# Kernel tuning notes

Hardware: AMD Instinct MI355X
Metric: run time of the kernel (lower is better)

Reference implementation:

```python
import jax, jax.numpy as jnp
import numpy as np

N_NODES = 100000
N_EDGES = 800000

def setup_inputs() -> dict:
    key = jax.random.key(0)
    ks = jax.random.split(key, 8)
    x = jax.random.normal(ks[0], (N_NODES, 500), dtype=jnp.float32)
    edge_index = jax.random.randint(ks[1], (2, N_EDGES), 0, N_NODES, dtype=jnp.int64)
    s = lambda k, shape, fan_in: jax.random.normal(k, shape, jnp.float32) / np.sqrt(fan_in)
    return {
        "x": x,
        "edge_index": edge_index,
        "W1_l": s(ks[2], (500, 20), 500),
        "W1_r": s(ks[3], (500, 20), 500),
        "b1": jnp.zeros((20,), jnp.float32),
        "W2_l": s(ks[4], (20, 3), 20),
        "W2_r": s(ks[5], (20, 3), 20),
        "b2": jnp.zeros((3,), jnp.float32),
    }

def _sage_conv(x, src, dst, W_l, W_r, b, deg_inv):
    # mean-aggregate neighbor features (x_j = x[src]) at dst, PyG default 'mean'
    agg = jax.ops.segment_sum(x[src], dst, num_segments=x.shape[0])  # [N, F]
    agg = agg * deg_inv[:, None]
    return agg @ W_l + b + x @ W_r

def reference(x, edge_index, W1_l, W1_r, b1, W2_l, W2_r, b2):
    src, dst = edge_index[0], edge_index[1]
    deg = jax.ops.segment_sum(jnp.ones_like(dst, dtype=x.dtype), dst, num_segments=x.shape[0])
    deg_inv = 1.0 / jnp.maximum(deg, 1.0)
    h = _sage_conv(x, src, dst, W1_l, W1_r, b1, deg_inv)
    h = jax.nn.relu(h)
    # F.dropout(p=0.5, training=self.training): identity in eval mode
    out = _sage_conv(h, src, dst, W2_l, W2_r, b2, deg_inv)
    return out
```

## Files before the change

kernel.cpp:

```cpp
#include <hip/hip_runtime.h>

#define F_IN  500
#define F_HID 20
#define F_OUT 3
#define KT    16
#define NT    3
#define PAD   32

typedef __attribute__((ext_vector_type(8))) short short8;
typedef __attribute__((ext_vector_type(4))) float v4f;

__device__ __forceinline__ unsigned f2bf(float f) {
    unsigned u = __float_as_uint(f);
    u = u + 0x7fffu + ((u >> 16) & 1u);
    return u >> 16;
}
__device__ __forceinline__ float bf2f(unsigned h) {
    return __uint_as_float(h << 16);
}

__device__ __forceinline__ void gload16(const void* g, void* l) {
    __builtin_amdgcn_global_load_lds((const __attribute__((address_space(1))) void*)g,
                                     (__attribute__((address_space(3))) void*)l, 16, 0, 0);
}

__device__ __forceinline__ void cvt8(const float4 p, const float4 q, short8& hi, short8& lo) {
    float vf[8] = {p.x, p.y, p.z, p.w, q.x, q.y, q.z, q.w};
    union { unsigned u[4]; short8 s; } H, L;
#pragma unroll
    for (int t = 0; t < 4; ++t) {
        unsigned u0 = __float_as_uint(vf[2*t]);
        unsigned u1 = __float_as_uint(vf[2*t+1]);
        unsigned r0 = u0 + 0x7fffu + ((u0 >> 16) & 1u);
        unsigned r1 = u1 + 0x7fffu + ((u1 >> 16) & 1u);
        float f0 = __uint_as_float(r0 & 0xffff0000u);
        float f1 = __uint_as_float(r1 & 0xffff0000u);
        float d0 = vf[2*t]   - f0;
        float d1 = vf[2*t+1] - f1;
        unsigned s0 = __float_as_uint(d0); s0 = s0 + 0x7fffu + ((s0 >> 16) & 1u);
        unsigned s1 = __float_as_uint(d1); s1 = s1 + 0x7fffu + ((s1 >> 16) & 1u);
        H.u[t] = (r0 >> 16) | (r1 & 0xffff0000u);
        L.u[t] = (s0 >> 16) | (s1 & 0xffff0000u);
    }
    hi = H.s; lo = L.s;
}

__global__ void k_init(const float* __restrict__ W1l, const float* __restrict__ W1r,
                       unsigned short* __restrict__ Bhi, unsigned short* __restrict__ Blo,
                       int* __restrict__ deg, int NZ4) {
    int b = blockIdx.x;
    int tid = threadIdx.x;
    if (b < (KT * NT * 64) / 256) {
        int i = b * 256 + tid;
        int lane = i & 63;
        int ntk  = i >> 6;
        int nt   = ntk % NT;
        int kt   = ntk / NT;
        int n     = nt * 16 + (lane & 15);
        int kbase = kt * 32 + (lane >> 4) * 8;
#pragma unroll
        for (int j = 0; j < 8; ++j) {
            int k = kbase + j;
            float w = 0.f;
            if (k < F_IN && n < 2 * F_HID)
                w = (n < F_HID) ? W1l[k * F_HID + n] : W1r[k * F_HID + (n - F_HID)];
            unsigned h = f2bf(w);
            Bhi[(size_t)i * 8 + j] = (unsigned short)h;
            Blo[(size_t)i * 8 + j] = (unsigned short)f2bf(w - bf2f(h));
        }
    } else {
        int i = (b - (KT * NT * 64) / 256) * 256 + tid;
        if (i < NZ4) ((int4*)deg)[i] = make_int4(0, 0, 0, 0);
    }
}

__global__ __launch_bounds__(256) void k_gemm_fill(const float* __restrict__ x,
        const unsigned short* __restrict__ Bhi, const unsigned short* __restrict__ Blo,
        float* __restrict__ yl, float* __restrict__ yr,
        const int* __restrict__ src, const int* __restrict__ dst,
        int* __restrict__ deg, int* __restrict__ csr,
        int N, int E, int GB) {
    __shared__ __align__(16) unsigned char lds[2 * 16384];
    if ((int)blockIdx.x >= GB) {
        int e0 = (((int)blockIdx.x - GB) * 256 + (int)threadIdx.x) * 4;
        if (e0 >= E) return;
        if (e0 + 3 < E) {
            int4 d4 = *(const int4*)(dst + e0);
            int4 s4 = *(const int4*)(src + e0);
            int p;
            p = atomicAdd(&deg[d4.x], 1); if (p < PAD) csr[(size_t)d4.x * PAD + p] = s4.x;
            p = atomicAdd(&deg[d4.y], 1); if (p < PAD) csr[(size_t)d4.y * PAD + p] = s4.y;
            p = atomicAdd(&deg[d4.z], 1); if (p < PAD) csr[(size_t)d4.z * PAD + p] = s4.z;
            p = atomicAdd(&deg[d4.w], 1); if (p < PAD) csr[(size_t)d4.w * PAD + p] = s4.w;
        } else {
            for (int e = e0; e < E; ++e) {
                int dn = dst[e];
                int p = atomicAdd(&deg[dn], 1);
                if (p < PAD) csr[(size_t)dn * PAD + p] = src[e];
            }
        }
        return;
    }
    const int tid  = threadIdx.x;
    const int lane = tid & 63;
    const int wv   = tid >> 6;
    const int fr   = lane & 15;
    const int kq   = lane >> 4;
    const int row0 = blockIdx.x * 64;

    int xrow[2], xcol[2];
#pragma unroll
    for (int cc = 0; cc < 2; ++cc) {
        int idx = (2 * wv + cc) * 64 + lane;
        int row = idx >> 3;
        int p   = idx & 7;
        int grow = row0 + row; if (grow > N - 1) grow = N - 1;
        xrow[cc] = grow;
        xcol[cc] = (p ^ (row & 7)) << 2;
    }
    const unsigned short* bsrcH = Bhi + (size_t)(wv % 3) * 512 + (size_t)lane * 8;
    const unsigned short* bsrcL = Blo + (size_t)(wv % 3) * 512 + (size_t)lane * 8;

#define STAGE(b, kt) do {                                                          \
        unsigned char* buf_ = lds + (b) * 16384;                                   \
        int k0_ = (kt) * 32 + xcol[0]; if (k0_ > 496) k0_ = 496;                   \
        int k1_ = (kt) * 32 + xcol[1]; if (k1_ > 496) k1_ = 496;                   \
        gload16(x + (size_t)xrow[0] * F_IN + k0_, buf_ + (2 * wv + 0) * 1024);     \
        gload16(x + (size_t)xrow[1] * F_IN + k1_, buf_ + (2 * wv + 1) * 1024);     \
        gload16(bsrcH + (size_t)(kt) * 1536, buf_ + 8192  + wv * 1024);            \
        gload16(bsrcL + (size_t)(kt) * 1536, buf_ + 12288 + wv * 1024);            \
    } while (0)

    v4f acc[NT];
#pragma unroll
    for (int nt = 0; nt < NT; ++nt) acc[nt] = (v4f){0.f, 0.f, 0.f, 0.f};

    const int arow  = wv * 16 + fr;
    const int abase = arow * 128;
    const int s0 = ((2 * kq)     ^ (arow & 7)) << 4;
    const int s1 = ((2 * kq + 1) ^ (arow & 7)) << 4;

    STAGE(0, 0);
    __syncthreads();

#pragma unroll
    for (int kt = 0; kt < KT; ++kt) {
        const int cb = kt & 1;
        if (kt + 1 < KT) STAGE(cb ^ 1, kt + 1);
        unsigned char* buf = lds + cb * 16384;
        float4 a0 = *(const float4*)(buf + abase + s0);
        float4 a1 = *(const float4*)(buf + abase + s1);
        short8 Ah, Al;
        cvt8(a0, a1, Ah, Al);
#pragma unroll
        for (int nt = 0; nt < NT; ++nt) {
            short8 Bh = *(const short8*)(buf + 8192  + nt * 1024 + lane * 16);
            short8 Bl = *(const short8*)(buf + 12288 + nt * 1024 + lane * 16);
            acc[nt] = __builtin_amdgcn_mfma_f32_16x16x32_bf16(Ah, Bh, acc[nt], 0, 0, 0);
            acc[nt] = __builtin_amdgcn_mfma_f32_16x16x32_bf16(Ah, Bl, acc[nt], 0, 0, 0);
            acc[nt] = __builtin_amdgcn_mfma_f32_16x16x32_bf16(Al, Bh, acc[nt], 0, 0, 0);
        }
        __syncthreads();
    }
#undef STAGE

    int rbase = row0 + wv * 16 + kq * 4;
#pragma unroll
    for (int nt = 0; nt < NT; ++nt) {
        int col = nt * 16 + fr;
        if (col < 2 * F_HID) {
#pragma unroll
            for (int rg = 0; rg < 4; ++rg) {
                int grow = rbase + rg;
                if (grow < N) {
                    if (col < F_HID) yl[(size_t)grow * 32 + col] = acc[nt][rg];
                    else             yr[(size_t)grow * F_HID + (col - F_HID)] = acc[nt][rg];
                }
            }
        }
    }
}

__global__ __launch_bounds__(256) void k_agg_l1(
        const int* __restrict__ deg, const int* __restrict__ csr,
        const float* __restrict__ yl, const float* __restrict__ yr,
        const float* __restrict__ b1, const float* __restrict__ W2l,
        const float* __restrict__ W2r,
        float* __restrict__ zl4, float* __restrict__ zr, int N) {
    int t = blockIdx.x * blockDim.x + threadIdx.x;
    int n = t >> 3;
    int g = t & 7;
    if (n >= N) return;
    int d   = min(deg[n], PAD);
    size_t beg = (size_t)n * PAD;
    float4 a = make_float4(0.f, 0.f, 0.f, 0.f);
    if (g < 5) {
        int j = 0;
        for (; j + 1 < d; j += 2) {
            int s0 = csr[beg + j];
            int s1 = csr[beg + j + 1];
            float4 v0 = *(const float4*)(yl + (size_t)s0 * 32 + g * 4);
            float4 v1 = *(const float4*)(yl + (size_t)s1 * 32 + g * 4);
            a.x += v0.x; a.y += v0.y; a.z += v0.z; a.w += v0.w;
            a.x += v1.x; a.y += v1.y; a.z += v1.z; a.w += v1.w;
        }
        if (j < d) {
            int s0 = csr[beg + j];
            float4 v0 = *(const float4*)(yl + (size_t)s0 * 32 + g * 4);
            a.x += v0.x; a.y += v0.y; a.z += v0.z; a.w += v0.w;
        }
    }
    float di = 1.0f / fmaxf((float)d, 1.0f);
    float pl0 = 0.f, pl1 = 0.f, pl2 = 0.f, pr0 = 0.f, pr1 = 0.f, pr2 = 0.f;
    if (g < 5) {
        float4 bb = *(const float4*)(b1 + g * 4);
        float4 rr = *(const float4*)(yr + (size_t)n * F_HID + g * 4);
        float h0 = fmaxf(a.x * di + bb.x + rr.x, 0.f);
        float h1 = fmaxf(a.y * di + bb.y + rr.y, 0.f);
        float h2 = fmaxf(a.z * di + bb.z + rr.z, 0.f);
        float h3 = fmaxf(a.w * di + bb.w + rr.w, 0.f);
        const float* wl = W2l + g * 4 * F_OUT;
        const float* wr = W2r + g * 4 * F_OUT;
        pl0 = h0 * wl[0] + h1 * wl[3] + h2 * wl[6] + h3 * wl[9];
        pl1 = h0 * wl[1] + h1 * wl[4] + h2 * wl[7] + h3 * wl[10];
        pl2 = h0 * wl[2] + h1 * wl[5] + h2 * wl[8] + h3 * wl[11];
        pr0 = h0 * wr[0] + h1 * wr[3] + h2 * wr[6] + h3 * wr[9];
        pr1 = h0 * wr[1] + h1 * wr[4] + h2 * wr[7] + h3 * wr[10];
        pr2 = h0 * wr[2] + h1 * wr[5] + h2 * wr[8] + h3 * wr[11];
    }
#pragma unroll
    for (int m = 4; m >= 1; m >>= 1) {
        pl0 += __shfl_xor(pl0, m);
        pl1 += __shfl_xor(pl1, m);
        pl2 += __shfl_xor(pl2, m);
        pr0 += __shfl_xor(pr0, m);
        pr1 += __shfl_xor(pr1, m);
        pr2 += __shfl_xor(pr2, m);
    }
    if (g == 0) {
        *(float4*)(zl4 + (size_t)n * 4) = make_float4(pl0, pl1, pl2, 0.f);
        zr[(size_t)n * 3 + 0] = pr0;
        zr[(size_t)n * 3 + 1] = pr1;
        zr[(size_t)n * 3 + 2] = pr2;
    }
}

__global__ void k_agg2_final(const int* __restrict__ deg, const int* __restrict__ csr,
                             const float* __restrict__ zl4, const float* __restrict__ zr,
                             const float* __restrict__ b2, float* __restrict__ out, int N) {
    int n = blockIdx.x * blockDim.x + threadIdx.x;
    if (n >= N) return;
    int d   = min(deg[n], PAD);
    size_t beg = (size_t)n * PAD;
    float a0 = 0.f, a1 = 0.f, a2 = 0.f;
    int j = 0;
    for (; j + 1 < d; j += 2) {
        int s0 = csr[beg + j];
        int s1 = csr[beg + j + 1];
        float4 z0 = *(const float4*)(zl4 + (size_t)s0 * 4);
        float4 z1 = *(const float4*)(zl4 + (size_t)s1 * 4);
        a0 += z0.x; a1 += z0.y; a2 += z0.z;
        a0 += z1.x; a1 += z1.y; a2 += z1.z;
    }
    if (j < d) {
        int s0 = csr[beg + j];
        float4 z0 = *(const float4*)(zl4 + (size_t)s0 * 4);
        a0 += z0.x; a1 += z0.y; a2 += z0.z;
    }
    float di = 1.0f / fmaxf((float)d, 1.0f);
    out[(size_t)n * F_OUT + 0] = a0 * di + b2[0] + zr[(size_t)n * 3 + 0];
    out[(size_t)n * F_OUT + 1] = a1 * di + b2[1] + zr[(size_t)n * 3 + 1];
    out[(size_t)n * F_OUT + 2] = a2 * di + b2[2] + zr[(size_t)n * 3 + 2];
}

extern "C" void kernel_launch(void* const* d_in, const int* in_sizes, int n_in,
                              void* d_out, int out_size, void* d_ws, size_t ws_size,
                              hipStream_t stream) {
    const float* x   = (const float*)d_in[0];
    const int*   ei  = (const int*)d_in[1];
    const float* W1l = (const float*)d_in[2];
    const float* W1r = (const float*)d_in[3];
    const float* b1  = (const float*)d_in[4];
    const float* W2l = (const float*)d_in[5];
    const float* W2r = (const float*)d_in[6];
    const float* b2  = (const float*)d_in[7];
    float* out = (float*)d_out;

    const int N = in_sizes[0] / F_IN;
    const int E = in_sizes[1] / 2;
    const int* src = ei;
    const int* dst = ei + E;

    int*   wsi  = (int*)d_ws;
    int*   deg  = wsi;
    int*   csr  = deg + ((N + 3) & ~3);
    float* yl   = (float*)(csr + (size_t)N * PAD);
    float* yr   = yl + (size_t)N * 32;
    float* zl4  = yr + (size_t)N * F_HID;
    float* zr   = zl4 + (size_t)N * 4;
    unsigned short* Bhi = (unsigned short*)(zr + (size_t)N * F_OUT);
    unsigned short* Blo = Bhi + (size_t)KT * NT * 64 * 8;

    const int B   = 256;
    const int PB  = (KT * NT * 64) / B;
    const int NZ4 = (N + 3) / 4;
    const int ZB  = (NZ4 + B - 1) / B;
    const int GB  = (N + 63) / 64;
    const int FB  = (E / 4 + B - 1) / B;

    k_init      <<<PB + ZB, B, 0, stream>>>(W1l, W1r, Bhi, Blo, deg, NZ4);
    k_gemm_fill <<<GB + FB, B, 0, stream>>>(x, Bhi, Blo, yl, yr, src, dst, deg, csr, N, E, GB);
    k_agg_l1    <<<((size_t)N * 8 + B - 1) / B, B, 0, stream>>>(deg, csr, yl, yr, b1, W2l, W2r, zl4, zr, N);
    k_agg2_final<<<(N + B - 1) / B, B, 0, stream>>>(deg, csr, zl4, zr, b2, out, N);
}
```

Baseline: 363.1 us.

## Interleave GEMM and CSR-fill blocks; split neighbor gathers across lanes in aggregations

The fused GEMM/CSR-fill launch now interleaves its blocks, two GEMM blocks for every fill block, instead of placing all fill blocks after the GEMM blocks. The aim is to overlap atomic-heavy CSR construction with the compute-bound GEMM. Layer-1 aggregation now gives each of 8 lanes a different neighbor, loads the full 20-wide row, and reduces with 20 shuffles per step. The layer-2 projection then runs only on lane 0. Layer-2 aggregation moves from one thread per node to 8 lanes per node with a shuffle reduction, which exposes more memory parallelism in both gathers at the cost of more registers and shuffles.

```diff
diff --git a/kernel.cpp b/kernel.cpp
--- a/kernel.cpp
+++ b/kernel.cpp
@@ -79,10 +79,15 @@
         float* __restrict__ yl, float* __restrict__ yr,
         const int* __restrict__ src, const int* __restrict__ dst,
         int* __restrict__ deg, int* __restrict__ csr,
-        int N, int E, int GB) {
+        int N, int E, int GB, int FB) {
     __shared__ __align__(16) unsigned char lds[2 * 16384];
-    if ((int)blockIdx.x >= GB) {
-        int e0 = (((int)blockIdx.x - GB) * 256 + (int)threadIdx.x) * 4;
+    const int bid   = (int)blockIdx.x;
+    const int third = bid / 3;
+    const int rem   = bid - third * 3;
+    if (rem == 2) {
+        int fb = third;
+        if (fb >= FB) return;
+        int e0 = (fb * 256 + (int)threadIdx.x) * 4;
         if (e0 >= E) return;
         if (e0 + 3 < E) {
             int4 d4 = *(const int4*)(dst + e0);
@@ -101,12 +106,14 @@
         }
         return;
     }
+    const int gb = third * 2 + rem;
+    if (gb >= GB) return;
     const int tid  = threadIdx.x;
     const int lane = tid & 63;
     const int wv   = tid >> 6;
     const int fr   = lane & 15;
     const int kq   = lane >> 4;
-    const int row0 = blockIdx.x * 64;
+    const int row0 = gb * 64;
 
     int xrow[2], xcol[2];
 #pragma unroll
@@ -193,84 +200,80 @@
     if (n >= N) return;
     int d   = min(deg[n], PAD);
     size_t beg = (size_t)n * PAD;
-    float4 a = make_float4(0.f, 0.f, 0.f, 0.f);
-    if (g < 5) {
-        int j = 0;
-        for (; j + 1 < d; j += 2) {
-            int s0 = csr[beg + j];
-            int s1 = csr[beg + j + 1];
-            float4 v0 = *(const float4*)(yl + (size_t)s0 * 32 + g * 4);
-            float4 v1 = *(const float4*)(yl + (size_t)s1 * 32 + g * 4);
-            a.x += v0.x; a.y += v0.y; a.z += v0.z; a.w += v0.w;
-            a.x += v1.x; a.y += v1.y; a.z += v1.z; a.w += v1.w;
-        }
-        if (j < d) {
-            int s0 = csr[beg + j];
-            float4 v0 = *(const float4*)(yl + (size_t)s0 * 32 + g * 4);
-            a.x += v0.x; a.y += v0.y; a.z += v0.z; a.w += v0.w;
-        }
-    }
-    float di = 1.0f / fmaxf((float)d, 1.0f);
-    float pl0 = 0.f, pl1 = 0.f, pl2 = 0.f, pr0 = 0.f, pr1 = 0.f, pr2 = 0.f;
-    if (g < 5) {
-        float4 bb = *(const float4*)(b1 + g * 4);
-        float4 rr = *(const float4*)(yr + (size_t)n * F_HID + g * 4);
-        float h0 = fmaxf(a.x * di + bb.x + rr.x, 0.f);
-        float h1 = fmaxf(a.y * di + bb.y + rr.y, 0.f);
-        float h2 = fmaxf(a.z * di + bb.z + rr.z, 0.f);
-        float h3 = fmaxf(a.w * di + bb.w + rr.w, 0.f);
-        const float* wl = W2l + g * 4 * F_OUT;
-        const float* wr = W2r + g * 4 * F_OUT;
-        pl0 = h0 * wl[0] + h1 * wl[3] + h2 * wl[6] + h3 * wl[9];
-        pl1 = h0 * wl[1] + h1 * wl[4] + h2 * wl[7] + h3 * wl[10];
-        pl2 = h0 * wl[2] + h1 * wl[5] + h2 * wl[8] + h3 * wl[11];
-        pr0 = h0 * wr[0] + h1 * wr[3] + h2 * wr[6] + h3 * wr[9];
-        pr1 = h0 * wr[1] + h1 * wr[4] + h2 * wr[7] + h3 * wr[10];
-        pr2 = h0 * wr[2] + h1 * wr[5] + h2 * wr[8] + h3 * wr[11];
+    float aa[F_HID];
+#pragma unroll
+    for (int c = 0; c < F_HID; ++c) aa[c] = 0.f;
+    for (int j = g; j < d; j += 8) {
+        int s = csr[beg + j];
+        const float4* p = (const float4*)(yl + (size_t)s * 32);
+#pragma unroll
+        for (int q = 0; q < 5; ++q) {
+            float4 v = p[q];
+            aa[4*q+0] += v.x; aa[4*q+1] += v.y; aa[4*q+2] += v.z; aa[4*q+3] += v.w;
+        }
     }
 #pragma unroll
     for (int m = 4; m >= 1; m >>= 1) {
-        pl0 += __shfl_xor(pl0, m);
-        pl1 += __shfl_xor(pl1, m);
-        pl2 += __shfl_xor(pl2, m);
-        pr0 += __shfl_xor(pr0, m);
-        pr1 += __shfl_xor(pr1, m);
-        pr2 += __shfl_xor(pr2, m);
+#pragma unroll
+        for (int c = 0; c < F_HID; ++c) aa[c] += __shfl_xor(aa[c], m);
     }
     if (g == 0) {
-        *(float4*)(zl4 + (size_t)n * 4) = make_float4(pl0, pl1, pl2, 0.f);
-        zr[(size_t)n * 3 + 0] = pr0;
-        zr[(size_t)n * 3 + 1] = pr1;
-        zr[(size_t)n * 3 + 2] = pr2;
-    }
-}
-
-__global__ void k_agg2_final(const int* __restrict__ deg, const int* __restrict__ csr,
-                             const float* __restrict__ zl4, const float* __restrict__ zr,
-                             const float* __restrict__ b2, float* __restrict__ out, int N) {
-    int n = blockIdx.x * blockDim.x + threadIdx.x;
+        float di = 1.0f / fmaxf((float)d, 1.0f);
+        const float4* pr = (const float4*)(yr + (size_t)n * F_HID);
+        float h[F_HID];
+#pragma unroll
+        for (int q = 0; q < 5; ++q) {
+            float4 r = pr[q];
+            h[4*q+0] = fmaxf(aa[4*q+0] * di + b1[4*q+0] + r.x, 0.f);
+            h[4*q+1] = fmaxf(aa[4*q+1] * di + b1[4*q+1] + r.y, 0.f);
+            h[4*q+2] = fmaxf(aa[4*q+2] * di + b1[4*q+2] + r.z, 0.f);
+            h[4*q+3] = fmaxf(aa[4*q+3] * di + b1[4*q+3] + r.w, 0.f);
+        }
+        float zlo[F_OUT] = {0.f, 0.f, 0.f};
+        float zro[F_OUT] = {0.f, 0.f, 0.f};
+#pragma unroll
+        for (int c = 0; c < F_HID; ++c) {
+#pragma unroll
+            for (int o = 0; o < F_OUT; ++o) {
+                zlo[o] += h[c] * W2l[c * F_OUT + o];
+                zro[o] += h[c] * W2r[c * F_OUT + o];
+            }
+        }
+        *(float4*)(zl4 + (size_t)n * 4) = make_float4(zlo[0], zlo[1], zlo[2], 0.f);
+        zr[(size_t)n * 3 + 0] = zro[0];
+        zr[(size_t)n * 3 + 1] = zro[1];
+        zr[(size_t)n * 3 + 2] = zro[2];
+    }
+}
+
+__global__ __launch_bounds__(256) void k_agg2_final(
+        const int* __restrict__ deg, const int* __restrict__ csr,
+        const float* __restrict__ zl4, const float* __restrict__ zr,
+        const float* __restrict__ b2, float* __restrict__ out, int N) {
+    int t = blockIdx.x * blockDim.x + threadIdx.x;
+    int n = t >> 3;
+    int g = t & 7;
     if (n >= N) return;
     int d   = min(deg[n], PAD);
     size_t beg = (size_t)n * PAD;
     float a0 = 0.f, a1 = 0.f, a2 = 0.f;
-    int j = 0;
-    for (; j + 1 < d; j += 2) {
-        int s0 = csr[beg + j];
-        int s1 = csr[beg + j + 1];
-        float4 z0 = *(const float4*)(zl4 + (size_t)s0 * 4);
-        float4 z1 = *(const float4*)(zl4 + (size_t)s1 * 4);
-        a0 += z0.x; a1 += z0.y; a2 += z0.z;
-        a0 += z1.x; a1 += z1.y; a2 += z1.z;
-    }
-    if (j < d) {
-        int s0 = csr[beg + j];
-        float4 z0 = *(const float4*)(zl4 + (size_t)s0 * 4);
-        a0 += z0.x; a1 += z0.y; a2 += z0.z;
-    }
-    float di = 1.0f / fmaxf((float)d, 1.0f);
-    out[(size_t)n * F_OUT + 0] = a0 * di + b2[0] + zr[(size_t)n * 3 + 0];
-    out[(size_t)n * F_OUT + 1] = a1 * di + b2[1] + zr[(size_t)n * 3 + 1];
-    out[(size_t)n * F_OUT + 2] = a2 * di + b2[2] + zr[(size_t)n * 3 + 2];
+    for (int j = g; j < d; j += 8) {
+        int s = csr[beg + j];
+        float4 z = *(const float4*)(zl4 + (size_t)s * 4);
+        a0 += z.x; a1 += z.y; a2 += z.z;
+    }
+#pragma unroll
+    for (int m = 4; m >= 1; m >>= 1) {
+        a0 += __shfl_xor(a0, m);
+        a1 += __shfl_xor(a1, m);
+        a2 += __shfl_xor(a2, m);
+    }
+    if (g == 0) {
+        float di = 1.0f / fmaxf((float)d, 1.0f);
+        out[(size_t)n * F_OUT + 0] = a0 * di + b2[0] + zr[(size_t)n * 3 + 0];
+        out[(size_t)n * F_OUT + 1] = a1 * di + b2[1] + zr[(size_t)n * 3 + 1];
+        out[(size_t)n * F_OUT + 2] = a2 * di + b2[2] + zr[(size_t)n * 3 + 2];
+    }
 }
 
 extern "C" void kernel_launch(void* const* d_in, const int* in_sizes, int n_in,
@@ -307,9 +310,10 @@
     const int ZB  = (NZ4 + B - 1) / B;
     const int GB  = (N + 63) / 64;
     const int FB  = (E / 4 + B - 1) / B;
+    const int TB  = 3 * FB;
 
     k_init      <<<PB + ZB, B, 0, stream>>>(W1l, W1r, Bhi, Blo, deg, NZ4);
-    k_gemm_fill <<<GB + FB, B, 0, stream>>>(x, Bhi, Blo, yl, yr, src, dst, deg, csr, N, E, GB);
+    k_gemm_fill <<<TB, B, 0, stream>>>(x, Bhi, Blo, yl, yr, src, dst, deg, csr, N, E, GB, FB);
     k_agg_l1    <<<((size_t)N * 8 + B - 1) / B, B, 0, stream>>>(deg, csr, yl, yr, b1, W2l, W2r, zl4, zr, N);
-    k_agg2_final<<<(N + B - 1) / B, B, 0, stream>>>(deg, csr, zl4, zr, b2, out, N);
-}
+    k_agg2_final<<<((size_t)N * 8 + B - 1) / B, B, 0, stream>>>(deg, csr, zl4, zr, b2, out, N);
+}
```

Result: no change. 367.0 us (+1.1%).
